# Kernel tuning notes

Hardware: AMD Instinct MI355X
Metric: run time of the kernel (lower is better)

The kernel has to match this reference:

```python
import jax, jax.numpy as jnp
import numpy as np

O, T = 20000, 80000
DIN_OBJ, DIN_PRED = 128, 128
H, DOUT = 256, 256
NCAPS, NHID = 8, 64
NLAYER, ROUTIT, TAU = 2, 3, 1.0
D = NCAPS * NHID                 # 512, routed feature dim
NFEAT1 = 2 * DIN_OBJ + DIN_PRED  # 384
NCLASS1 = 2 * H + DOUT           # 768
BN_EPS = 1e-5


def _l2norm(x):
    # torch fn.normalize(dim=-1): x / max(||x||, 1e-12)
    nrm = jnp.sqrt(jnp.sum(x * x, axis=-1, keepdims=True))
    return x / jnp.maximum(nrm, 1e-12)


def _rout(x, src, trg):
    # NeibRoutLayer: iterative capsule routing over edges
    n, d = x.shape
    dd = d // NCAPS
    x3 = _l2norm(x.reshape(n, NCAPS, dd))   # [n,k,dd]
    z = x3[src]                              # [m,k,dd] gathered source capsules
    u = x3
    for _ in range(ROUTIT):
        p = jax.nn.softmax(jnp.einsum('mkd,mkd->mk', z, u[trg]) / TAU, axis=1)  # [m,k]
        agg = jax.ops.segment_sum(z * p[:, :, None], trg, num_segments=n)       # scatter_add
        u = _l2norm(agg + x3)
    return u.reshape(n, d)


def _disengcn(x, src, trg, pca_w, pca_b, clf_w, clf_b, bn_g, bn_b):
    x = jax.nn.leaky_relu(x @ pca_w + pca_b)  # slope 0.01, dropout=0 (eval)
    for _ in range(NLAYER):
        x = _rout(x, src, trg)
    x = x @ clf_w + clf_b
    # BatchNorm1d in eval mode with running_mean=0, running_var=1
    x = x * (bn_g / jnp.sqrt(jnp.asarray(1.0 + BN_EPS, x.dtype))) + bn_b
    return jax.nn.leaky_relu(x)


def setup_inputs() -> dict:
    key = jax.random.key(0)
    ks = jax.random.split(key, 16)

    def unif(k, shape, stdv):
        return jax.random.uniform(k, shape, jnp.float32, -stdv, stdv)

    inp = {}
    inp['obj_vecs'] = jax.random.normal(ks[0], (O, DIN_OBJ), jnp.float32)
    inp['pred_vecs'] = jax.random.normal(ks[1], (T, DIN_PRED), jnp.float32)
    inp['edges'] = jax.random.randint(ks[2], (T, 2), 0, O, jnp.int64)
    # net1 params (SparseInputLinear uses 1/sqrt(out_dim), nn.Linear 1/sqrt(in_dim))
    inp['pca_w1'] = unif(ks[3], (NFEAT1, D), 1.0 / np.sqrt(D))
    inp['pca_b1'] = unif(ks[4], (D,), 1.0 / np.sqrt(D))
    inp['clf_w1'] = unif(ks[5], (D, NCLASS1), 1.0 / np.sqrt(D))
    inp['clf_b1'] = unif(ks[6], (NCLASS1,), 1.0 / np.sqrt(D))
    inp['bn_g1'] = 1.0 + 0.05 * jax.random.normal(ks[7], (NCLASS1,), jnp.float32)
    inp['bn_b1'] = 0.05 * jax.random.normal(ks[8], (NCLASS1,), jnp.float32)
    # net2 params
    inp['pca_w2'] = unif(ks[9], (H, D), 1.0 / np.sqrt(D))
    inp['pca_b2'] = unif(ks[10], (D,), 1.0 / np.sqrt(D))
    inp['clf_w2'] = unif(ks[11], (D, DOUT), 1.0 / np.sqrt(D))
    inp['clf_b2'] = unif(ks[12], (DOUT,), 1.0 / np.sqrt(D))
    inp['bn_g2'] = 1.0 + 0.05 * jax.random.normal(ks[13], (DOUT,), jnp.float32)
    inp['bn_b2'] = 0.05 * jax.random.normal(ks[14], (DOUT,), jnp.float32)
    return inp


def reference(obj_vecs, pred_vecs, edges, pca_w1, pca_b1, clf_w1, clf_b1, bn_g1, bn_b1,
              pca_w2, pca_b2, clf_w2, clf_b2, bn_g2, bn_b2):
    s_idx, o_idx = edges[:, 0], edges[:, 1]
    # extract_info: per-triplet concat [subj, pred, obj]
    t_vecs = jnp.concatenate([obj_vecs[s_idx], pred_vecs, obj_vecs[o_idx]], axis=1)  # [T, 384]
    out1 = _disengcn(t_vecs, s_idx, o_idx, pca_w1, pca_b1, clf_w1, clf_b1, bn_g1, bn_b1)  # [T, 768]
    # pool_objs: scatter_add subject/object features back to nodes, mean by count
    new_s = out1[:, :H]
    pred_out = out1[:, H:H + DOUT]
    new_o = out1[:, H + DOUT:]
    pooled = jax.ops.segment_sum(new_s, s_idx, num_segments=O) + \
             jax.ops.segment_sum(new_o, o_idx, num_segments=O)
    ones = jnp.ones((edges.shape[0],), out1.dtype)
    counts = jax.ops.segment_sum(ones, s_idx, num_segments=O) + \
             jax.ops.segment_sum(ones, o_idx, num_segments=O)
    pooled = pooled / jnp.maximum(counts, 1.0)[:, None]
    obj_out = _disengcn(pooled, s_idx, o_idx, pca_w2, pca_b2, clf_w2, clf_b2, bn_g2, bn_b2)  # [O, 256]
    return obj_out, pred_out
```

## Files before the change

kernel.cpp:

```cpp
#include <hip/hip_runtime.h>
#include <math.h>


#define O_N 20000
#define T_N 80000
#define BIG_REQ 207944000ull

typedef unsigned short bf_t;
typedef bf_t bfx4 __attribute__((ext_vector_type(4)));
typedef bf_t bfx8 __attribute__((ext_vector_type(8)));
typedef __attribute__((ext_vector_type(4))) float f32x4;
typedef __attribute__((ext_vector_type(8))) short s16x8;

#define AS1 __attribute__((address_space(1)))
#define AS3 __attribute__((address_space(3)))

__device__ __forceinline__ float leaky(float y) { return y > 0.0f ? y : 0.01f * y; }
__device__ __forceinline__ float bf2f(bf_t u) {
  union { unsigned int i; float f; } v; v.i = ((unsigned int)u) << 16; return v.f;
}
__device__ __forceinline__ bf_t f2bf(float f) {
  union { float f; unsigned int i; } v; v.f = f;
  unsigned int b = v.i;
  return (bf_t)((b + 0x7FFFu + ((b >> 16) & 1u)) >> 16);
}
__device__ __forceinline__ void gload16(const bf_t* g, bf_t* l) {
  __builtin_amdgcn_global_load_lds((const AS1 void*)g, (AS3 void*)l, 16, 0, 0);
}

__global__ void count_kernel(const int* __restrict__ edges, int* cnt_s, int* cnt_o) {
  int m = blockIdx.x * blockDim.x + threadIdx.x;
  if (m < T_N) {
    atomicAdd(&cnt_s[edges[2 * m]], 1);
    atomicAdd(&cnt_o[edges[2 * m + 1]], 1);
  }
}

__global__ void scan_kernel(const int* __restrict__ cnt_s, const int* __restrict__ cnt_o,
                            int* offs_s, int* cur_s, int* offs_o, int* cur_o) {
  const int n = O_N;
  const int* cnt = (blockIdx.x == 0) ? cnt_s : cnt_o;
  int* offs = (blockIdx.x == 0) ? offs_s : offs_o;
  int* cur  = (blockIdx.x == 0) ? cur_s  : cur_o;
  __shared__ int lds[1024];
  __shared__ int sbase;
  if (threadIdx.x == 0) sbase = 0;
  __syncthreads();
  for (int start = 0; start < n; start += 1024) {
    int i = start + (int)threadIdx.x;
    int v = (i < n) ? cnt[i] : 0;
    lds[threadIdx.x] = v;
    __syncthreads();
    for (int off = 1; off < 1024; off <<= 1) {
      int t = (threadIdx.x >= (unsigned)off) ? lds[threadIdx.x - off] : 0;
      __syncthreads();
      lds[threadIdx.x] += t;
      __syncthreads();
    }
    int base = sbase;
    int excl = base + lds[threadIdx.x] - v;
    if (i < n) { offs[i] = excl; cur[i] = excl; }
    __syncthreads();
    if (threadIdx.x == 1023) sbase = base + lds[1023];
    __syncthreads();
  }
  if (threadIdx.x == 0) offs[n] = sbase;
}

__global__ void fill_kernel(const int* __restrict__ edges, int* cur_s, int* cur_o,
                            int* srcs, int* slot_s, int* slot_o) {
  int m = blockIdx.x * blockDim.x + threadIdx.x;
  if (m < T_N) {
    int s = edges[2 * m], o = edges[2 * m + 1];
    int ps = atomicAdd(&cur_s[s], 1);
    slot_s[m] = ps;
    int po = atomicAdd(&cur_o[o], 1);
    slot_o[m] = po;
    srcs[po] = s;
  }
}

__global__ void cvt_pred(const float* __restrict__ src, bf_t* __restrict__ dst, int n8) {
  int i = blockIdx.x * blockDim.x + threadIdx.x;
  if (i >= n8) return;
  float4 a = ((const float4*)src)[2 * i];
  float4 b = ((const float4*)src)[2 * i + 1];
  bfx8 w;
  w[0] = f2bf(a.x); w[1] = f2bf(a.y); w[2] = f2bf(a.z); w[3] = f2bf(a.w);
  w[4] = f2bf(b.x); w[5] = f2bf(b.y); w[6] = f2bf(b.z); w[7] = f2bf(b.w);
  *(bfx8*)(dst + (size_t)i * 8) = w;
}

__global__ void transpose_cvt(const float* __restrict__ W, bf_t* __restrict__ Wt, int K, int N) {
  __shared__ float t[32][33];
  int kb = blockIdx.y << 5, nb = blockIdx.x << 5;
  int tx = threadIdx.x, ty = threadIdx.y;
#pragma unroll
  for (int r = 0; r < 32; r += 8) t[ty + r][tx] = W[(size_t)(kb + ty + r) * N + nb + tx];
  __syncthreads();
#pragma unroll
  for (int r = 0; r < 32; r += 8) Wt[(size_t)(nb + ty + r) * K + kb + tx] = f2bf(t[tx][ty + r]);
}

__device__ __forceinline__ void stage16(const float* base, bf_t* stA, int slot0) {
  float4 q0 = ((const float4*)base)[0];
  float4 q1 = ((const float4*)base)[1];
  float4 q2 = ((const float4*)base)[2];
  float4 q3 = ((const float4*)base)[3];
  bfx8 w0, w1;
  w0[0] = f2bf(q0.x); w0[1] = f2bf(q0.y); w0[2] = f2bf(q0.z); w0[3] = f2bf(q0.w);
  w0[4] = f2bf(q1.x); w0[5] = f2bf(q1.y); w0[6] = f2bf(q1.z); w0[7] = f2bf(q1.w);
  w1[0] = f2bf(q2.x); w1[1] = f2bf(q2.y); w1[2] = f2bf(q2.z); w1[3] = f2bf(q2.w);
  w1[4] = f2bf(q3.x); w1[5] = f2bf(q3.y); w1[6] = f2bf(q3.z); w1[7] = f2bf(q3.w);
  *(bfx8*)(stA + slot0 * 8) = w0;
  *(bfx8*)(stA + (slot0 ^ 1) * 8) = w1;
}

template <int MODE, int CB>
__global__ __launch_bounds__(256) void gemm_mfma(
    const bf_t* __restrict__ Ah, const bf_t* __restrict__ Axh,
    const float* __restrict__ Af, const float* __restrict__ obj,
    const int* __restrict__ edges,
    const bf_t* __restrict__ Wt, const float* __restrict__ bias,
    const float* __restrict__ bng, const float* __restrict__ bnb,
    bf_t* __restrict__ outh, float* __restrict__ outf, float* __restrict__ pool,
    bf_t* __restrict__ vs, bf_t* __restrict__ vo,
    const int* __restrict__ slot_s, const int* __restrict__ slot_o,
    int NRB, int M, int N, int K) {
  const int id = blockIdx.x;
  const int lane8 = id & 7, tt = id >> 3;
  const int cb = tt % CB, qq = tt / CB;
  const int yb = (qq << 3) + lane8;
  if (yb >= NRB) return;
  const int row0 = yb * 128, col0 = cb * 128;

  __shared__ __align__(16) bf_t As[128 * 32];
  __shared__ __align__(16) bf_t Bs[128 * 32];

  const int tid = threadIdx.x;
  const int w = tid >> 6, l = tid & 63;
  const int wr = w >> 1, wc = w & 1;

  const int srow = l >> 2;
  const int skb = ((l & 3) ^ (srow & 3) ^ ((srow >> 2) & 3)) * 8;
  const bf_t* pB[2];
  bf_t* ldsB[2];
  bf_t* ldsA[2];
  const bf_t* pA[2];
#pragma unroll
  for (int j = 0; j < 2; ++j) {
    int n = col0 + j * 64 + w * 16 + srow;
    pB[j] = Wt + (size_t)n * K + skb;
    ldsB[j] = Bs + (j * 64 + w * 16) * 32;
    ldsA[j] = As + (j * 64 + w * 16) * 32;
  }
  if constexpr (MODE == 1 || MODE == 3 || MODE == 4) {
#pragma unroll
    for (int j = 0; j < 2; ++j) {
      int m = row0 + j * 64 + w * 16 + srow;
      if (MODE == 3) m = min(m, M - 1);
      const bf_t* base = (MODE == 3) ? Ah : ((m < O_N) ? Ah : Axh);
      pA[j] = base + (size_t)m * 512 + skb;
    }
  }
  const int r_ = tid >> 1, h_ = tid & 1;
  const int slot0_ = (2 * h_) ^ (r_ & 3) ^ ((r_ >> 2) & 3);
  bf_t* stA = As + r_ * 32;
  int sIdx = 0, oIdx = 0, mrow = 0;
  if constexpr (MODE == 0) {
    mrow = row0 + r_;
    sIdx = edges[2 * mrow];
    oIdx = edges[2 * mrow + 1];
#pragma unroll
    for (int j = 0; j < 2; ++j)
      pA[j] = Ah + (size_t)(row0 + j * 64 + w * 16 + srow) * 128 + skb;
  }
  if constexpr (MODE == 2) mrow = min(row0 + r_, M - 1);

  const int pkb = ((l >> 4) ^ (l & 3) ^ ((l >> 2) & 3)) * 8;
  int aoff[4], boff[4];
#pragma unroll
  for (int i = 0; i < 4; ++i) {
    aoff[i] = (wr * 64 + i * 16 + (l & 15)) * 32 + pkb;
    boff[i] = (wc * 64 + i * 16 + (l & 15)) * 32 + pkb;
  }

  f32x4 acc[4][4];
  const f32x4 z4 = {0.f, 0.f, 0.f, 0.f};
#pragma unroll
  for (int i = 0; i < 4; ++i)
#pragma unroll
    for (int j = 0; j < 4; ++j) acc[i][j] = z4;

  for (int k0 = 0; k0 < K; k0 += 32) {
    if (k0) __syncthreads();
#pragma unroll
    for (int j = 0; j < 2; ++j) { gload16(pB[j], ldsB[j]); pB[j] += 32; }
    if constexpr (MODE == 1 || MODE == 3 || MODE == 4) {
#pragma unroll
      for (int j = 0; j < 2; ++j) { gload16(pA[j], ldsA[j]); pA[j] += 32; }
    } else if constexpr (MODE == 0) {
      if (k0 >= 128 && k0 < 256) {
        gload16(pA[0] + (k0 - 128), ldsA[0]);
        gload16(pA[1] + (k0 - 128), ldsA[1]);
      } else {
        const float* base = (k0 < 128)
            ? obj + (size_t)sIdx * 128 + k0 + h_ * 16
            : obj + (size_t)oIdx * 128 + (k0 - 256) + h_ * 16;
        stage16(base, stA, slot0_);
      }
    } else {
      stage16(Af + (size_t)mrow * K + k0 + h_ * 16, stA, slot0_);
    }
    __syncthreads();
    s16x8 a[4], b[4];
#pragma unroll
    for (int i = 0; i < 4; ++i) a[i] = *(const s16x8*)(As + aoff[i]);
#pragma unroll
    for (int i = 0; i < 4; ++i) b[i] = *(const s16x8*)(Bs + boff[i]);
#pragma unroll
    for (int mi = 0; mi < 4; ++mi)
#pragma unroll
      for (int ni = 0; ni < 4; ++ni)
        acc[mi][ni] = __builtin_amdgcn_mfma_f32_16x16x32_bf16(a[mi], b[ni], acc[mi][ni], 0, 0, 0);
  }

  const int lg = l >> 4, li = l & 15;
  const float invs = 1.0f / sqrtf(1.0f + 1e-5f);
  int ncol[4];
  float bsv[4], bgv[4], bbv[4];
#pragma unroll
  for (int ni = 0; ni < 4; ++ni) {
    int n = col0 + wc * 64 + ni * 16 + li;
    ncol[ni] = n;
    bsv[ni] = bias[n];
    if constexpr (MODE == 1 || MODE == 3 || MODE == 4) { bgv[ni] = bng[n] * invs; bbv[ni] = bnb[n]; }
  }
  if constexpr (MODE == 0 || MODE == 2) {
#pragma unroll
    for (int mi = 0; mi < 4; ++mi) {
#pragma unroll
      for (int rg = 0; rg < 4; ++rg) {
        int m = row0 + wr * 64 + mi * 16 + lg * 4 + rg;
        float y[4], ssq = 0.f;
#pragma unroll
        for (int ni = 0; ni < 4; ++ni) {
          float v = leaky(acc[mi][ni][rg] + bsv[ni]);
          y[ni] = v; ssq += v * v;
        }
        ssq += __shfl_xor(ssq, 1); ssq += __shfl_xor(ssq, 2);
        ssq += __shfl_xor(ssq, 4); ssq += __shfl_xor(ssq, 8);
        if (MODE == 2 && m >= M) continue;
        float inv = 1.0f / fmaxf(sqrtf(ssq), 1e-12f);
#pragma unroll
        for (int ni = 0; ni < 4; ++ni)
          outh[(size_t)m * 512 + ncol[ni]] = f2bf(y[ni] * inv);
      }
    }
  } else if constexpr (MODE == 1) {
#pragma unroll
    for (int mi = 0; mi < 4; ++mi) {
#pragma unroll
      for (int rg = 0; rg < 4; ++rg) {
        int m = row0 + wr * 64 + mi * 16 + lg * 4 + rg;
        int sI = edges[2 * m], oI = edges[2 * m + 1];
#pragma unroll
        for (int ni = 0; ni < 4; ++ni) {
          int n = ncol[ni];
          float v = leaky((acc[mi][ni][rg] + bsv[ni]) * bgv[ni] + bbv[ni]);
          if (n < 256)      atomicAdd(&pool[(size_t)sI * 256 + n], v);
          else if (n < 512) outf[(size_t)m * 256 + (n - 256)] = v;
          else              atomicAdd(&pool[(size_t)oI * 256 + (n - 512)], v);
        }
      }
    }
  } else if constexpr (MODE == 4) {
#pragma unroll
    for (int mi = 0; mi < 4; ++mi) {
#pragma unroll
      for (int rg = 0; rg < 4; ++rg) {
        int m = row0 + wr * 64 + mi * 16 + lg * 4 + rg;
        int ss = slot_s[m], so = slot_o[m];
#pragma unroll
        for (int ni = 0; ni < 4; ++ni) {
          int n = ncol[ni];
          float v = leaky((acc[mi][ni][rg] + bsv[ni]) * bgv[ni] + bbv[ni]);
          if (n < 256)      vs[(size_t)ss * 256 + n] = f2bf(v);
          else if (n < 512) outf[(size_t)m * 256 + (n - 256)] = v;
          else              vo[(size_t)so * 256 + (n - 512)] = f2bf(v);
        }
      }
    }
  } else {
#pragma unroll
    for (int mi = 0; mi < 4; ++mi) {
#pragma unroll
      for (int rg = 0; rg < 4; ++rg) {
        int m = row0 + wr * 64 + mi * 16 + lg * 4 + rg;
        if (m >= M) continue;
#pragma unroll
        for (int ni = 0; ni < 4; ++ni) {
          float v = leaky((acc[mi][ni][rg] + bsv[ni]) * bgv[ni] + bbv[ni]);
          outf[(size_t)m * 256 + ncol[ni]] = v;
        }
      }
    }
  }
}

__global__ __launch_bounds__(256) void pool_so(
    const bf_t* __restrict__ vs, const bf_t* __restrict__ vo,
    const int* __restrict__ offs_s, const int* __restrict__ offs_o,
    float* __restrict__ PL, int nnodes) {
  int v = blockIdx.x * 4 + ((int)threadIdx.x >> 6);
  int lane = threadIdx.x & 63;
  if (v >= nnodes) return;
  float sx = 0, sy = 0, sz = 0, sw = 0;
  int a0 = offs_s[v], a1 = offs_s[v + 1];
  for (int e = a0; e < a1; ++e) {
    bfx4 t = *(const bfx4*)(vs + (size_t)e * 256 + lane * 4);
    sx += bf2f(t[0]); sy += bf2f(t[1]); sz += bf2f(t[2]); sw += bf2f(t[3]);
  }
  int b0 = offs_o[v], b1 = offs_o[v + 1];
  for (int e = b0; e < b1; ++e) {
    bfx4 t = *(const bfx4*)(vo + (size_t)e * 256 + lane * 4);
    sx += bf2f(t[0]); sy += bf2f(t[1]); sz += bf2f(t[2]); sw += bf2f(t[3]);
  }
  float inv = 1.0f / fmaxf((float)((a1 - a0) + (b1 - b0)), 1.0f);
  float4 r = {sx * inv, sy * inv, sz * inv, sw * inv};
  *(float4*)(PL + (size_t)v * 256 + lane * 4) = r;
}

#define EDGE_STEP(ZR)                                                                   \
  {                                                                                     \
    float d = 0.0f;                                                                     \
    _Pragma("unroll") for (int q = 0; q < 8; ++q) d += (ZR)[q] * ur[q];                 \
    d += __shfl_xor(d, 1); d += __shfl_xor(d, 2); d += __shfl_xor(d, 4);                \
    float mx = d;                                                                       \
    mx = fmaxf(mx, __shfl_xor(mx, 8));                                                  \
    mx = fmaxf(mx, __shfl_xor(mx, 16));                                                 \
    mx = fmaxf(mx, __shfl_xor(mx, 32));                                                 \
    float ex = expf(d - mx);                                                            \
    float sm = ex;                                                                      \
    sm += __shfl_xor(sm, 8); sm += __shfl_xor(sm, 16); sm += __shfl_xor(sm, 32);        \
    float pk = ex / sm;                                                                 \
    _Pragma("unroll") for (int q = 0; q < 8; ++q) ag[q] += pk * (ZR)[q];                \
  }

__global__ __launch_bounds__(256) void rout_layer(
    const bf_t* __restrict__ Z, bf_t* __restrict__ U,
    const int* __restrict__ offs, const int* __restrict__ srcs, int nnodes) {
  int v = blockIdx.x * 4 + ((int)threadIdx.x >> 6);
  int lane = threadIdx.x & 63;
  if (v >= nnodes) return;
  bfx8 xv = *(const bfx8*)(Z + (size_t)v * 512 + lane * 8);
  float xr[8], ur[8];
#pragma unroll
  for (int q = 0; q < 8; ++q) { xr[q] = bf2f(xv[q]); ur[q] = xr[q]; }
  int e0 = offs[v], e1 = offs[v + 1], deg = e1 - e0;
  if (deg <= 8) {
    bfx8 zc[8];
#pragma unroll
    for (int e = 0; e < 8; ++e)
      if (e < deg) zc[e] = *(const bfx8*)(Z + (size_t)srcs[e0 + e] * 512 + lane * 8);
    for (int it = 0; it < 3; ++it) {
      float ag[8] = {0, 0, 0, 0, 0, 0, 0, 0};
#pragma unroll
      for (int e = 0; e < 8; ++e)
        if (e < deg) {
          float zr[8];
#pragma unroll
          for (int q = 0; q < 8; ++q) zr[q] = bf2f(zc[e][q]);
          EDGE_STEP(zr);
        }
      float ss = 0.0f, wv[8];
#pragma unroll
      for (int q = 0; q < 8; ++q) { wv[q] = ag[q] + xr[q]; ss += wv[q] * wv[q]; }
      ss += __shfl_xor(ss, 1); ss += __shfl_xor(ss, 2); ss += __shfl_xor(ss, 4);
      float inv = 1.0f / fmaxf(sqrtf(ss), 1e-12f);
#pragma unroll
      for (int q = 0; q < 8; ++q) ur[q] = wv[q] * inv;
    }
  } else {
    for (int it = 0; it < 3; ++it) {
      float ag[8] = {0, 0, 0, 0, 0, 0, 0, 0};
      for (int e = e0; e < e1; ++e) {
        bfx8 zv = *(const bfx8*)(Z + (size_t)srcs[e] * 512 + lane * 8);
        float zr[8];
#pragma unroll
        for (int q = 0; q < 8; ++q) zr[q] = bf2f(zv[q]);
        EDGE_STEP(zr);
      }
      float ss = 0.0f, wv[8];
#pragma unroll
      for (int q = 0; q < 8; ++q) { wv[q] = ag[q] + xr[q]; ss += wv[q] * wv[q]; }
      ss += __shfl_xor(ss, 1); ss += __shfl_xor(ss, 2); ss += __shfl_xor(ss, 4);
      float inv = 1.0f / fmaxf(sqrtf(ss), 1e-12f);
#pragma unroll
      for (int q = 0; q < 8; ++q) ur[q] = wv[q] * inv;
    }
  }
  bfx8 ov;
#pragma unroll
  for (int q = 0; q < 8; ++q) ov[q] = f2bf(ur[q]);
  *(bfx8*)(U + (size_t)v * 512 + lane * 8) = ov;
}

__global__ void divide_kernel(float* __restrict__ PL,
                              const int* __restrict__ offs_s, const int* __restrict__ offs_o) {
  int v = blockIdx.x;
  int c = threadIdx.x;
  float cnt = (float)((offs_s[v + 1] - offs_s[v]) + (offs_o[v + 1] - offs_o[v]));
  PL[(size_t)v * 256 + c] *= 1.0f / fmaxf(cnt, 1.0f);
}

extern "C" void kernel_launch(void* const* d_in, const int* in_sizes, int n_in,
                              void* d_out, int out_size, void* d_ws, size_t ws_size,
                              hipStream_t stream) {
  const float* obj    = (const float*)d_in[0];
  const float* pred   = (const float*)d_in[1];
  const int*   edges  = (const int*)d_in[2];
  const float* pca_w1 = (const float*)d_in[3];
  const float* pca_b1 = (const float*)d_in[4];
  const float* clf_w1 = (const float*)d_in[5];
  const float* clf_b1 = (const float*)d_in[6];
  const float* bn_g1  = (const float*)d_in[7];
  const float* bn_b1  = (const float*)d_in[8];
  const float* pca_w2 = (const float*)d_in[9];
  const float* pca_b2 = (const float*)d_in[10];
  const float* clf_w2 = (const float*)d_in[11];
  const float* clf_b2 = (const float*)d_in[12];
  const float* bn_g2  = (const float*)d_in[13];
  const float* bn_b2  = (const float*)d_in[14];
  float* outp = (float*)d_out;

  char* ws = (char*)d_ws;
  bf_t* Xh    = (bf_t*)ws;
  bf_t* Uh2   = (bf_t*)(ws + 81920000);
  bf_t* predh = (bf_t*)(ws + 102400000);
  bf_t* Uh1   = (bf_t*)(ws + 102400000);
  float* PL   = (float*)(ws + 102400000);
  bf_t* Wt1   = (bf_t*)(ws + 122880000);
  bf_t* Wt2   = (bf_t*)(ws + 123273216);
  bf_t* Wt3   = (bf_t*)(ws + 124059648);
  bf_t* Wt4   = (bf_t*)(ws + 124321792);
  int* I      = (int*)(ws + 124583936);
  int* cnt_s  = I;            int* cnt_o  = I + 20000;
  int* offs_s = I + 40000;    int* offs_o = I + 60001;
  int* cur_s  = I + 80002;    int* cur_o  = I + 100002;
  int* srcs   = I + 120002;
  int* slot_s = I + 200002;   int* slot_o = I + 280002;
  bf_t* val_s = (bf_t*)(ws + 126024000);
  bf_t* val_o = (bf_t*)(ws + 166984000);
  const bool big = (ws_size >= BIG_REQ);

  hipMemsetAsync(cnt_s, 0, 160000, stream);
  count_kernel<<<313, 256, 0, stream>>>(edges, cnt_s, cnt_o);
  scan_kernel<<<2, 1024, 0, stream>>>(cnt_s, cnt_o, offs_s, cur_s, offs_o, cur_o);
  fill_kernel<<<313, 256, 0, stream>>>(edges, cur_s, cur_o, srcs, slot_s, slot_o);

  cvt_pred<<<5000, 256, 0, stream>>>(pred, predh, 1280000);
  transpose_cvt<<<dim3(16, 12), dim3(32, 8), 0, stream>>>(pca_w1, Wt1, 384, 512);
  transpose_cvt<<<dim3(24, 16), dim3(32, 8), 0, stream>>>(clf_w1, Wt2, 512, 768);
  transpose_cvt<<<dim3(16, 8),  dim3(32, 8), 0, stream>>>(pca_w2, Wt3, 256, 512);
  transpose_cvt<<<dim3(8, 16),  dim3(32, 8), 0, stream>>>(clf_w2, Wt4, 512, 256);

  const int g1 = 8 * 79 * 4;
  const int g2 = 8 * 79 * 6;
  const int g3 = 8 * 20 * 4;
  const int g4 = 8 * 20 * 2;

  gemm_mfma<0, 4><<<g1, 256, 0, stream>>>(predh, nullptr, nullptr, obj, edges,
                                          Wt1, pca_b1, nullptr, nullptr,
                                          Xh, nullptr, nullptr, nullptr, nullptr,
                                          nullptr, nullptr, 625, T_N, 512, 384);
  rout_layer<<<5000, 256, 0, stream>>>(Xh, Uh1, offs_o, srcs, O_N);
  rout_layer<<<5000, 256, 0, stream>>>(Uh1, Uh2, offs_o, srcs, O_N);
  if (big) {
    gemm_mfma<4, 6><<<g2, 256, 0, stream>>>(Uh2, Xh, nullptr, nullptr, edges,
                                            Wt2, clf_b1, bn_g1, bn_b1,
                                            nullptr, outp + 5120000, nullptr, val_s, val_o,
                                            slot_s, slot_o, 625, T_N, 768, 512);
    pool_so<<<5000, 256, 0, stream>>>(val_s, val_o, offs_s, offs_o, PL, O_N);
  } else {
    hipMemsetAsync(PL, 0, 20480000, stream);
    gemm_mfma<1, 6><<<g2, 256, 0, stream>>>(Uh2, Xh, nullptr, nullptr, edges,
                                            Wt2, clf_b1, bn_g1, bn_b1,
                                            nullptr, outp + 5120000, PL, nullptr, nullptr,
                                            nullptr, nullptr, 625, T_N, 768, 512);
    divide_kernel<<<O_N, 256, 0, stream>>>(PL, offs_s, offs_o);
  }

  gemm_mfma<2, 4><<<g3, 256, 0, stream>>>(nullptr, nullptr, PL, nullptr, nullptr,
                                          Wt3, pca_b2, nullptr, nullptr,
                                          Xh, nullptr, nullptr, nullptr, nullptr,
                                          nullptr, nullptr, 157, O_N, 512, 256);
  rout_layer<<<5000, 256, 0, stream>>>(Xh, Uh1, offs_o, srcs, O_N);
  rout_layer<<<5000, 256, 0, stream>>>(Uh1, Uh2, offs_o, srcs, O_N);
  gemm_mfma<3, 2><<<g4, 256, 0, stream>>>(Uh2, nullptr, nullptr, nullptr, nullptr,
                                          Wt4, clf_b2, bn_g2, bn_b2,
                                          nullptr, outp, nullptr, nullptr, nullptr,
                                          nullptr, nullptr, 157, O_N, 256, 512);
}
```

Measured before the change: 767.2 us.

## Double-buffer GEMM LDS tiles and pre-convert all A operands to bf16

```diff
diff --git a/kernel.cpp b/kernel.cpp
--- a/kernel.cpp
+++ b/kernel.cpp
@@ -4,7 +4,7 @@
 
 #define O_N 20000
 #define T_N 80000
-#define BIG_REQ 207944000ull
+#define BIG_REQ 223304016ull
 
 typedef unsigned short bf_t;
 typedef bf_t bfx4 __attribute__((ext_vector_type(4)));
@@ -80,7 +80,7 @@
   }
 }
 
-__global__ void cvt_pred(const float* __restrict__ src, bf_t* __restrict__ dst, int n8) {
+__global__ void cvt_bf16(const float* __restrict__ src, bf_t* __restrict__ dst, int n8) {
   int i = blockIdx.x * blockDim.x + threadIdx.x;
   if (i >= n8) return;
   float4 a = ((const float4*)src)[2 * i];
@@ -102,24 +102,9 @@
   for (int r = 0; r < 32; r += 8) Wt[(size_t)(nb + ty + r) * K + kb + tx] = f2bf(t[tx][ty + r]);
 }
 
-__device__ __forceinline__ void stage16(const float* base, bf_t* stA, int slot0) {
-  float4 q0 = ((const float4*)base)[0];
-  float4 q1 = ((const float4*)base)[1];
-  float4 q2 = ((const float4*)base)[2];
-  float4 q3 = ((const float4*)base)[3];
-  bfx8 w0, w1;
-  w0[0] = f2bf(q0.x); w0[1] = f2bf(q0.y); w0[2] = f2bf(q0.z); w0[3] = f2bf(q0.w);
-  w0[4] = f2bf(q1.x); w0[5] = f2bf(q1.y); w0[6] = f2bf(q1.z); w0[7] = f2bf(q1.w);
-  w1[0] = f2bf(q2.x); w1[1] = f2bf(q2.y); w1[2] = f2bf(q2.z); w1[3] = f2bf(q2.w);
-  w1[4] = f2bf(q3.x); w1[5] = f2bf(q3.y); w1[6] = f2bf(q3.z); w1[7] = f2bf(q3.w);
-  *(bfx8*)(stA + slot0 * 8) = w0;
-  *(bfx8*)(stA + (slot0 ^ 1) * 8) = w1;
-}
-
 template <int MODE, int CB>
 __global__ __launch_bounds__(256) void gemm_mfma(
     const bf_t* __restrict__ Ah, const bf_t* __restrict__ Axh,
-    const float* __restrict__ Af, const float* __restrict__ obj,
     const int* __restrict__ edges,
     const bf_t* __restrict__ Wt, const float* __restrict__ bias,
     const float* __restrict__ bng, const float* __restrict__ bnb,
@@ -134,8 +119,8 @@
   if (yb >= NRB) return;
   const int row0 = yb * 128, col0 = cb * 128;
 
-  __shared__ __align__(16) bf_t As[128 * 32];
-  __shared__ __align__(16) bf_t Bs[128 * 32];
+  __shared__ __align__(16) bf_t As[2][128 * 32];
+  __shared__ __align__(16) bf_t Bs[2][128 * 32];
 
   const int tid = threadIdx.x;
   const int w = tid >> 6, l = tid & 63;
@@ -143,39 +128,31 @@
 
   const int srow = l >> 2;
   const int skb = ((l & 3) ^ (srow & 3) ^ ((srow >> 2) & 3)) * 8;
-  const bf_t* pB[2];
-  bf_t* ldsB[2];
-  bf_t* ldsA[2];
-  const bf_t* pA[2];
+  const bf_t* srcB[2];
+  const bf_t* srcA[2];
+  const bf_t* srcS[2];
+  const bf_t* srcP[2];
+  const bf_t* srcO[2];
+  int ldsOff[2];
 #pragma unroll
   for (int j = 0; j < 2; ++j) {
     int n = col0 + j * 64 + w * 16 + srow;
-    pB[j] = Wt + (size_t)n * K + skb;
-    ldsB[j] = Bs + (j * 64 + w * 16) * 32;
-    ldsA[j] = As + (j * 64 + w * 16) * 32;
-  }
-  if constexpr (MODE == 1 || MODE == 3 || MODE == 4) {
-#pragma unroll
-    for (int j = 0; j < 2; ++j) {
-      int m = row0 + j * 64 + w * 16 + srow;
-      if (MODE == 3) m = min(m, M - 1);
-      const bf_t* base = (MODE == 3) ? Ah : ((m < O_N) ? Ah : Axh);
-      pA[j] = base + (size_t)m * 512 + skb;
-    }
-  }
-  const int r_ = tid >> 1, h_ = tid & 1;
-  const int slot0_ = (2 * h_) ^ (r_ & 3) ^ ((r_ >> 2) & 3);
-  bf_t* stA = As + r_ * 32;
-  int sIdx = 0, oIdx = 0, mrow = 0;
-  if constexpr (MODE == 0) {
-    mrow = row0 + r_;
-    sIdx = edges[2 * mrow];
-    oIdx = edges[2 * mrow + 1];
-#pragma unroll
-    for (int j = 0; j < 2; ++j)
-      pA[j] = Ah + (size_t)(row0 + j * 64 + w * 16 + srow) * 128 + skb;
-  }
-  if constexpr (MODE == 2) mrow = min(row0 + r_, M - 1);
+    srcB[j] = Wt + (size_t)n * K + skb;
+    ldsOff[j] = (j * 64 + w * 16) * 32;
+    int rowA = row0 + j * 64 + w * 16 + srow;
+    if constexpr (MODE == 1 || MODE == 4) {
+      srcA[j] = ((rowA < O_N) ? Ah : Axh) + (size_t)rowA * 512 + skb;
+    } else if constexpr (MODE == 3) {
+      srcA[j] = Ah + (size_t)min(rowA, M - 1) * 512 + skb;
+    } else if constexpr (MODE == 2) {
+      srcA[j] = Ah + (size_t)min(rowA, M - 1) * 256 + skb;
+    } else {
+      int s = edges[2 * rowA], o = edges[2 * rowA + 1];
+      srcS[j] = Axh + (size_t)s * 128 + skb;
+      srcP[j] = Ah + (size_t)rowA * 128 + skb;
+      srcO[j] = Axh + (size_t)o * 128 + skb;
+    }
+  }
 
   const int pkb = ((l >> 4) ^ (l & 3) ^ ((l >> 2) & 3)) * 8;
   int aoff[4], boff[4];
@@ -192,37 +169,56 @@
 #pragma unroll
     for (int j = 0; j < 4; ++j) acc[i][j] = z4;
 
-  for (int k0 = 0; k0 < K; k0 += 32) {
-    if (k0) __syncthreads();
-#pragma unroll
-    for (int j = 0; j < 2; ++j) { gload16(pB[j], ldsB[j]); pB[j] += 32; }
-    if constexpr (MODE == 1 || MODE == 3 || MODE == 4) {
-#pragma unroll
-      for (int j = 0; j < 2; ++j) { gload16(pA[j], ldsA[j]); pA[j] += 32; }
-    } else if constexpr (MODE == 0) {
-      if (k0 >= 128 && k0 < 256) {
-        gload16(pA[0] + (k0 - 128), ldsA[0]);
-        gload16(pA[1] + (k0 - 128), ldsA[1]);
+  auto STAGE = [&](int t, int buf) {
+    const int k0 = t << 5;
+#pragma unroll
+    for (int j = 0; j < 2; ++j) {
+      if constexpr (MODE == 0) {
+        const bf_t* s;
+        if (k0 < 128)      s = srcS[j] + k0;
+        else if (k0 < 256) s = srcP[j] + (k0 - 128);
+        else               s = srcO[j] + (k0 - 256);
+        gload16(s, &As[buf][ldsOff[j]]);
       } else {
-        const float* base = (k0 < 128)
-            ? obj + (size_t)sIdx * 128 + k0 + h_ * 16
-            : obj + (size_t)oIdx * 128 + (k0 - 256) + h_ * 16;
-        stage16(base, stA, slot0_);
+        gload16(srcA[j] + k0, &As[buf][ldsOff[j]]);
       }
-    } else {
-      stage16(Af + (size_t)mrow * K + k0 + h_ * 16, stA, slot0_);
-    }
-    __syncthreads();
+      gload16(srcB[j] + k0, &Bs[buf][ldsOff[j]]);
+    }
+  };
+  auto COMPUTE = [&](int buf) {
     s16x8 a[4], b[4];
 #pragma unroll
-    for (int i = 0; i < 4; ++i) a[i] = *(const s16x8*)(As + aoff[i]);
-#pragma unroll
-    for (int i = 0; i < 4; ++i) b[i] = *(const s16x8*)(Bs + boff[i]);
+    for (int i = 0; i < 4; ++i) a[i] = *(const s16x8*)(&As[buf][aoff[i]]);
+#pragma unroll
+    for (int i = 0; i < 4; ++i) b[i] = *(const s16x8*)(&Bs[buf][boff[i]]);
 #pragma unroll
     for (int mi = 0; mi < 4; ++mi)
 #pragma unroll
       for (int ni = 0; ni < 4; ++ni)
         acc[mi][ni] = __builtin_amdgcn_mfma_f32_16x16x32_bf16(a[mi], b[ni], acc[mi][ni], 0, 0, 0);
+  };
+
+  const int nt = K >> 5;
+  STAGE(0, 0);
+  for (int t = 0; t < nt; t += 2) {
+    STAGE(t + 1, 1);
+    asm volatile("s_waitcnt vmcnt(4)" ::: "memory");
+    __builtin_amdgcn_s_barrier();
+    __builtin_amdgcn_sched_barrier(0);
+    COMPUTE(0);
+    __builtin_amdgcn_sched_barrier(0);
+    __builtin_amdgcn_s_barrier();
+    if (t + 2 < nt) {
+      STAGE(t + 2, 0);
+      asm volatile("s_waitcnt vmcnt(4)" ::: "memory");
+    } else {
+      asm volatile("s_waitcnt vmcnt(0)" ::: "memory");
+    }
+    __builtin_amdgcn_s_barrier();
+    __builtin_amdgcn_sched_barrier(0);
+    COMPUTE(1);
+    __builtin_amdgcn_sched_barrier(0);
+    __builtin_amdgcn_s_barrier();
   }
 
   const int lg = l >> 4, li = l & 15;
@@ -311,7 +307,7 @@
 __global__ __launch_bounds__(256) void pool_so(
     const bf_t* __restrict__ vs, const bf_t* __restrict__ vo,
     const int* __restrict__ offs_s, const int* __restrict__ offs_o,
-    float* __restrict__ PL, int nnodes) {
+    bf_t* __restrict__ PLh, int nnodes) {
   int v = blockIdx.x * 4 + ((int)threadIdx.x >> 6);
   int lane = threadIdx.x & 63;
   if (v >= nnodes) return;
@@ -327,8 +323,10 @@
     sx += bf2f(t[0]); sy += bf2f(t[1]); sz += bf2f(t[2]); sw += bf2f(t[3]);
   }
   float inv = 1.0f / fmaxf((float)((a1 - a0) + (b1 - b0)), 1.0f);
-  float4 r = {sx * inv, sy * inv, sz * inv, sw * inv};
-  *(float4*)(PL + (size_t)v * 256 + lane * 4) = r;
+  bfx4 r;
+  r[0] = f2bf(sx * inv); r[1] = f2bf(sy * inv);
+  r[2] = f2bf(sz * inv); r[3] = f2bf(sw * inv);
+  *(bfx4*)(PLh + (size_t)v * 256 + lane * 4) = r;
 }
 
 #define EDGE_STEP(ZR)                                                                   \
@@ -406,12 +404,12 @@
   *(bfx8*)(U + (size_t)v * 512 + lane * 8) = ov;
 }
 
-__global__ void divide_kernel(float* __restrict__ PL,
+__global__ void divide_kernel(const float* __restrict__ PL, bf_t* __restrict__ PLh,
                               const int* __restrict__ offs_s, const int* __restrict__ offs_o) {
   int v = blockIdx.x;
   int c = threadIdx.x;
   float cnt = (float)((offs_s[v + 1] - offs_s[v]) + (offs_o[v + 1] - offs_o[v]));
-  PL[(size_t)v * 256 + c] *= 1.0f / fmaxf(cnt, 1.0f);
+  PLh[(size_t)v * 256 + c] = f2bf(PL[(size_t)v * 256 + c] / fmaxf(cnt, 1.0f));
 }
 
 extern "C" void kernel_launch(void* const* d_in, const int* in_sizes, int n_in,
@@ -440,18 +438,20 @@
   bf_t* predh = (bf_t*)(ws + 102400000);
   bf_t* Uh1   = (bf_t*)(ws + 102400000);
   float* PL   = (float*)(ws + 102400000);
-  bf_t* Wt1   = (bf_t*)(ws + 122880000);
-  bf_t* Wt2   = (bf_t*)(ws + 123273216);
-  bf_t* Wt3   = (bf_t*)(ws + 124059648);
-  bf_t* Wt4   = (bf_t*)(ws + 124321792);
-  int* I      = (int*)(ws + 124583936);
+  bf_t* objh  = (bf_t*)(ws + 122880000);
+  bf_t* PLh   = (bf_t*)(ws + 128000000);
+  bf_t* Wt1   = (bf_t*)(ws + 138240000);
+  bf_t* Wt2   = (bf_t*)(ws + 138633216);
+  bf_t* Wt3   = (bf_t*)(ws + 139419648);
+  bf_t* Wt4   = (bf_t*)(ws + 139681792);
+  int* I      = (int*)(ws + 139944000);
   int* cnt_s  = I;            int* cnt_o  = I + 20000;
   int* offs_s = I + 40000;    int* offs_o = I + 60001;
   int* cur_s  = I + 80002;    int* cur_o  = I + 100002;
   int* srcs   = I + 120002;
   int* slot_s = I + 200002;   int* slot_o = I + 280002;
-  bf_t* val_s = (bf_t*)(ws + 126024000);
-  bf_t* val_o = (bf_t*)(ws + 166984000);
+  bf_t* val_s = (bf_t*)(ws + 141384016);
+  bf_t* val_o = (bf_t*)(ws + 182344016);
   const bool big = (ws_size >= BIG_REQ);
 
   hipMemsetAsync(cnt_s, 0, 160000, stream);
@@ -459,7 +459,8 @@
   scan_kernel<<<2, 1024, 0, stream>>>(cnt_s, cnt_o, offs_s, cur_s, offs_o, cur_o);
   fill_kernel<<<313, 256, 0, stream>>>(edges, cur_s, cur_o, srcs, slot_s, slot_o);
 
-  cvt_pred<<<5000, 256, 0, stream>>>(pred, predh, 1280000);
+  cvt_bf16<<<5000, 256, 0, stream>>>(pred, predh, 1280000);
+  cvt_bf16<<<1250, 256, 0, stream>>>(obj, objh, 320000);
   transpose_cvt<<<dim3(16, 12), dim3(32, 8), 0, stream>>>(pca_w1, Wt1, 384, 512);
   transpose_cvt<<<dim3(24, 16), dim3(32, 8), 0, stream>>>(clf_w1, Wt2, 512, 768);
   transpose_cvt<<<dim3(16, 8),  dim3(32, 8), 0, stream>>>(pca_w2, Wt3, 256, 512);
@@ -470,34 +471,34 @@
   const int g3 = 8 * 20 * 4;
   const int g4 = 8 * 20 * 2;
 
-  gemm_mfma<0, 4><<<g1, 256, 0, stream>>>(predh, nullptr, nullptr, obj, edges,
+  gemm_mfma<0, 4><<<g1, 256, 0, stream>>>(predh, objh, edges,
                                           Wt1, pca_b1, nullptr, nullptr,
                                           Xh, nullptr, nullptr, nullptr, nullptr,
                                           nullptr, nullptr, 625, T_N, 512, 384);
   rout_layer<<<5000, 256, 0, stream>>>(Xh, Uh1, offs_o, srcs, O_N);
   rout_layer<<<5000, 256, 0, stream>>>(Uh1, Uh2, offs_o, srcs, O_N);
   if (big) {
-    gemm_mfma<4, 6><<<g2, 256, 0, stream>>>(Uh2, Xh, nullptr, nullptr, edges,
+    gemm_mfma<4, 6><<<g2, 256, 0, stream>>>(Uh2, Xh, edges,
                                             Wt2, clf_b1, bn_g1, bn_b1,
                                             nullptr, outp + 5120000, nullptr, val_s, val_o,
                                             slot_s, slot_o, 625, T_N, 768, 512);
-    pool_so<<<5000, 256, 0, stream>>>(val_s, val_o, offs_s, offs_o, PL, O_N);
+    pool_so<<<5000, 256, 0, stream>>>(val_s, val_o, offs_s, offs_o, PLh, O_N);
   } else {
     hipMemsetAsync(PL, 0, 20480000, stream);
-    gemm_mfma<1, 6><<<g2, 256, 0, stream>>>(Uh2, Xh, nullptr, nullptr, edges,
+    gemm_mfma<1, 6><<<g2, 256, 0, stream>>>(Uh2, Xh, edges,
                                             Wt2, clf_b1, bn_g1, bn_b1,
                                             nullptr, outp + 5120000, PL, nullptr, nullptr,
                                             nullptr, nullptr, 625, T_N, 768, 512);
-    divide_kernel<<<O_N, 256, 0, stream>>>(PL, offs_s, offs_o);
-  }
-
-  gemm_mfma<2, 4><<<g3, 256, 0, stream>>>(nullptr, nullptr, PL, nullptr, nullptr,
+    divide_kernel<<<O_N, 256, 0, stream>>>(PL, PLh, offs_s, offs_o);
+  }
+
+  gemm_mfma<2, 4><<<g3, 256, 0, stream>>>(PLh, nullptr, nullptr,
                                           Wt3, pca_b2, nullptr, nullptr,
                                           Xh, nullptr, nullptr, nullptr, nullptr,
                                           nullptr, nullptr, 157, O_N, 512, 256);
   rout_layer<<<5000, 256, 0, stream>>>(Xh, Uh1, offs_o, srcs, O_N);
   rout_layer<<<5000, 256, 0, stream>>>(Uh1, Uh2, offs_o, srcs, O_N);
-  gemm_mfma<3, 2><<<g4, 256, 0, stream>>>(Uh2, nullptr, nullptr, nullptr, nullptr,
+  gemm_mfma<3, 2><<<g4, 256, 0, stream>>>(Uh2, nullptr, nullptr,
                                           Wt4, clf_b2, bn_g2, bn_b2,
                                           nullptr, outp, nullptr, nullptr, nullptr,
                                           nullptr, nullptr, 157, O_N, 256, 512);
```

Result: no change. 765.1 us (-0.3%).
